# Kernel optimization log

Measured on AMD Instinct MI355X. Metric: run time of the kernel, lower is better.

## Reference

```python
import jax, jax.numpy as jnp
import numpy as np

IN_DIM, D, B, N = 6, 256, 2048, 100  # inner_dim=latent_dim=256, max_size=100


def _glorot(key, shape):
    fan = sum(shape)
    return jax.random.uniform(key, shape, jnp.float32, -1.0, 1.0) * np.sqrt(6.0 / fan)


def setup_inputs() -> dict:
    key = jax.random.key(0)
    ks = jax.random.split(key, 16)
    inp = {
        "x": jax.random.normal(ks[0], (B, N, IN_DIM), jnp.float32),
        "full": 1,
        "remap_w": _glorot(ks[1], (D, IN_DIM)),
        "remap_b": jnp.zeros((D,), jnp.float32),
    }
    for l in range(4):
        k = jax.random.split(ks[2 + l], 3)
        inp[f"w{l+1}"] = _glorot(k[0], (D, D))          # GATConv lin weight (bias=False)
        inp[f"as{l+1}"] = _glorot(k[1], (D,)) * 0.1      # att_src
        inp[f"ad{l+1}"] = _glorot(k[2], (D,)) * 0.1      # att_dst
        inp[f"b{l+1}"] = jnp.zeros((D,), jnp.float32)    # post-aggregation bias
    return inp


def _gat(h, w, a_src, a_dst, b):
    # Complete digraph with self-loops (full=True path) => dense softmax attention.
    g = jnp.einsum("bnd,od->bno", h, w)                  # [B,N,D] transformed nodes
    s_src = jnp.einsum("bno,o->bn", g, a_src)            # score of node as source j
    s_dst = jnp.einsum("bno,o->bn", g, a_dst)            # score of node as target i
    logits = jax.nn.leaky_relu(s_dst[:, :, None] + s_src[:, None, :], 0.2)  # [B,i,j]
    attn = jax.nn.softmax(logits, axis=-1)               # softmax over sources per target
    return jnp.einsum("bij,bjo->bio", attn, g) + b


def reference(x, full, remap_w, remap_b,
              w1, as1, ad1, b1, w2, as2, ad2, b2,
              w3, as3, ad3, b3, w4, as4, ad4, b4):
    h = jax.nn.relu(jnp.einsum("bni,oi->bno", x, remap_w) + remap_b)
    h = jax.nn.relu(_gat(h, w1, as1, ad1, b1) + h)
    h = jax.nn.relu(_gat(h, w2, as2, ad2, b2) + h)
    h = jax.nn.relu(_gat(h, w3, as3, ad3, b3) + h)
    h = _gat(h, w4, as4, ad4, b4)
    return h
```

## Files before the change

### kernel.cpp

```cpp
#include <hip/hip_runtime.h>
#include <hip/hip_bf16.h>


typedef __attribute__((ext_vector_type(8))) short bf16x8;
typedef __attribute__((ext_vector_type(4))) short bf16x4;
typedef __attribute__((ext_vector_type(4))) float f32x4;

__device__ __forceinline__ float bf2f(unsigned short u) {
    return __uint_as_float(((unsigned)u) << 16);
}
__device__ __forceinline__ short f2bfs(float f) {
    __hip_bfloat16 h = __float2bfloat16(f);
    return *reinterpret_cast<short*>(&h);
}

#define HS_OFF 0
#define GT_OFF 57344
#define P_OFF  122880
#define SS_OFF 151552
#define SD_OFF 152000
#define X_OFF  152448
#define SMEM_BYTES 154848

__device__ __forceinline__ int hs_addr(int row, int col) {
    return HS_OFF + row * 512 + ((col * 2) ^ ((row & 7) << 4));
}
__device__ __forceinline__ int gt_addr(int o, int n) {
    return GT_OFF + o * 256 + ((n * 2) ^ ((o & 7) << 4));
}
__device__ __forceinline__ int p_addr(int i, int j) {
    return P_OFF + i * 256 + ((j * 2) ^ ((i & 7) << 4));
}

struct LayerPtrs {
    const float* w[4];
    const float* bias[4];
};
struct PrepPtrs {
    const float* w[4];
    const float* as_[4];
    const float* ad_[4];
};

__global__ __launch_bounds__(256) void prep_kernel(PrepPtrs p, unsigned short* wsd) {
    const int l = blockIdx.x;
    const int d = threadIdx.x;
    __shared__ float As[256], Ad[256];
    As[d] = p.as_[l][d];
    Ad[d] = p.ad_[l][d];
    __syncthreads();
    const float* W = p.w[l];
    float s1 = 0.f, s2 = 0.f;
    for (int o = 0; o < 256; ++o) {
        float wv = W[o * 256 + d];
        s1 = fmaf(wv, As[o], s1);
        s2 = fmaf(wv, Ad[o], s2);
    }
    wsd[l * 512 + d]       = (unsigned short)f2bfs(s1);
    wsd[l * 512 + 256 + d] = (unsigned short)f2bfs(s2);
}

__global__ __launch_bounds__(512) void geom_kernel(
    const float* __restrict__ x,
    const float* __restrict__ remap_w,
    const float* __restrict__ remap_b,
    LayerPtrs lp,
    const unsigned short* __restrict__ wsd,
    float* __restrict__ out)
{
    extern __shared__ char smem[];
    const int tid  = threadIdx.x;
    const int lane = tid & 63;
    const int wv   = tid >> 6;
    const int c    = lane & 15;
    const int q    = lane >> 4;
    const int b    = blockIdx.x;

    for (int off = tid * 16; off < (P_OFF + 28672) - GT_OFF; off += 512 * 16) {
        *(f32x4*)(smem + GT_OFF + off) = f32x4{0.f, 0.f, 0.f, 0.f};
    }
    float* Xs = (float*)(smem + X_OFF);
    const float* xb = x + (size_t)b * 600;
    for (int s = tid; s < 600; s += 512) Xs[s] = xb[s];
    __syncthreads();

    {
        const int o = tid & 255, half = tid >> 8;
        float rw[6];
#pragma unroll
        for (int i = 0; i < 6; ++i) rw[i] = remap_w[o * 6 + i];
        const float rb = remap_b[o];
        for (int n = half * 56; n < half * 56 + 56; ++n) {
            float v = 0.f;
            if (n < 100) {
                v = rb;
#pragma unroll
                for (int i = 0; i < 6; ++i) v = fmaf(Xs[n * 6 + i], rw[i], v);
                v = fmaxf(v, 0.f);
            }
            *(unsigned short*)(smem + hs_addr(n, o)) = (unsigned short)f2bfs(v);
        }
    }

    float res[7][4][2];

    for (int l = 0; l < 4; ++l) {
        __syncthreads();
        const float* W = lp.w[l];
        const int nt0 = 2 * wv, nt1 = 2 * wv + 1;

        {
            bf16x8 wf0[8], wf1[8];
            const float* p0 = W + (nt0 * 16 + c) * 256 + q * 8;
            const float* p1 = W + (nt1 * 16 + c) * 256 + q * 8;
#pragma unroll
            for (int kk = 0; kk < 8; ++kk) {
                f32x4 lo0 = *(const f32x4*)(p0 + kk * 32);
                f32x4 hi0 = *(const f32x4*)(p0 + kk * 32 + 4);
                f32x4 lo1 = *(const f32x4*)(p1 + kk * 32);
                f32x4 hi1 = *(const f32x4*)(p1 + kk * 32 + 4);
                bf16x8 w0, w1;
#pragma unroll
                for (int j = 0; j < 4; ++j) {
                    w0[j]     = f2bfs(lo0[j]);
                    w0[4 + j] = f2bfs(hi0[j]);
                    w1[j]     = f2bfs(lo1[j]);
                    w1[4 + j] = f2bfs(hi1[j]);
                }
                wf0[kk] = w0;
                wf1[kk] = w1;
            }
            for (int mt = 0; mt < 7; ++mt) {
                f32x4 a0e = {0,0,0,0}, a0o = {0,0,0,0}, a1e = {0,0,0,0}, a1o = {0,0,0,0};
#pragma unroll
                for (int kk = 0; kk < 8; kk += 2) {
                    bf16x8 afe = *(const bf16x8*)(smem + hs_addr(mt * 16 + c, kk * 32 + q * 8));
                    bf16x8 afo = *(const bf16x8*)(smem + hs_addr(mt * 16 + c, (kk + 1) * 32 + q * 8));
                    a0e = __builtin_amdgcn_mfma_f32_16x16x32_bf16(afe, wf0[kk],     a0e, 0, 0, 0);
                    a1e = __builtin_amdgcn_mfma_f32_16x16x32_bf16(afe, wf1[kk],     a1e, 0, 0, 0);
                    a0o = __builtin_amdgcn_mfma_f32_16x16x32_bf16(afo, wf0[kk + 1], a0o, 0, 0, 0);
                    a1o = __builtin_amdgcn_mfma_f32_16x16x32_bf16(afo, wf1[kk + 1], a1o, 0, 0, 0);
                }
                f32x4 a0 = a0e + a0o, a1 = a1e + a1o;
                bf16x4 g0, g1;
#pragma unroll
                for (int j = 0; j < 4; ++j) {
                    g0[j] = f2bfs(a0[j]);
                    g1[j] = f2bfs(a1[j]);
                }
                *(bf16x4*)(smem + gt_addr(nt0 * 16 + c, mt * 16 + q * 4)) = g0;
                *(bf16x4*)(smem + gt_addr(nt1 * 16 + c, mt * 16 + q * 4)) = g1;
            }
            if (wv < 7) {
                const unsigned short* wsp = wsd + l * 512 + q * 8;
                const unsigned short* wdp = wsp + 256;
                f32x4 sa = {0,0,0,0};
#pragma unroll
                for (int kk = 0; kk < 8; ++kk) {
                    bf16x8 af = *(const bf16x8*)(smem + hs_addr(wv * 16 + c, kk * 32 + q * 8));
                    bf16x8 bs = *(const bf16x8*)(wsp + kk * 32);
                    bf16x8 bd = *(const bf16x8*)(wdp + kk * 32);
                    bf16x8 bz = {0,0,0,0,0,0,0,0};
                    bf16x8 bb = (c == 0) ? bs : ((c == 1) ? bd : bz);
                    sa = __builtin_amdgcn_mfma_f32_16x16x32_bf16(af, bb, sa, 0, 0, 0);
                }
                if (c < 2) {
                    float* dst = (float*)(smem + (c == 0 ? SS_OFF : SD_OFF));
#pragma unroll
                    for (int j = 0; j < 4; ++j) dst[wv * 16 + q * 4 + j] = sa[j];
                }
            }
        }
        __syncthreads();

        {
            const int i = tid >> 2, sq = tid & 3;
            if (i < 100) {
                const float sd = ((float*)(smem + SD_OFF))[i];
                const float* Ssf = (const float*)(smem + SS_OFF);
                float vals[4][8];
                float mx = -1e30f;
#pragma unroll
                for (int t = 0; t < 4; ++t) {
                    const int blk = t * 4 + sq;
#pragma unroll
                    for (int e = 0; e < 8; ++e) {
                        const int j = blk * 8 + e;
                        float v;
                        if (j < 100) {
                            float z = sd + Ssf[j];
                            v = (z > 0.f) ? z : 0.2f * z;
                        } else {
                            v = -1e30f;
                        }
                        vals[t][e] = v;
                        mx = fmaxf(mx, v);
                    }
                }
                mx = fmaxf(mx, __shfl_xor(mx, 1, 4));
                mx = fmaxf(mx, __shfl_xor(mx, 2, 4));
                float sum = 0.f;
#pragma unroll
                for (int t = 0; t < 4; ++t)
#pragma unroll
                    for (int e = 0; e < 8; ++e) {
                        float ev = __expf(vals[t][e] - mx);
                        vals[t][e] = ev;
                        sum += ev;
                    }
                sum += __shfl_xor(sum, 1, 4);
                sum += __shfl_xor(sum, 2, 4);
                const float inv = 1.f / sum;
#pragma unroll
                for (int t = 0; t < 4; ++t) {
                    const int blk = t * 4 + sq;
                    bf16x8 pv;
#pragma unroll
                    for (int e = 0; e < 8; ++e) pv[e] = f2bfs(vals[t][e] * inv);
                    *(bf16x8*)(smem + p_addr(i, blk * 8)) = pv;
                }
            }
        }
        __syncthreads();

        {
            const float* bias = lp.bias[l];
            const float b0 = bias[nt0 * 16 + c];
            const float b1 = bias[nt1 * 16 + c];
#pragma unroll
            for (int mt = 0; mt < 7; ++mt) {
                f32x4 a0e = {0,0,0,0}, a0o = {0,0,0,0}, a1e = {0,0,0,0}, a1o = {0,0,0,0};
#pragma unroll
                for (int kk = 0; kk < 4; kk += 2) {
                    bf16x8 afe = *(const bf16x8*)(smem + p_addr(mt * 16 + c, kk * 32 + q * 8));
                    bf16x8 afo = *(const bf16x8*)(smem + p_addr(mt * 16 + c, (kk + 1) * 32 + q * 8));
                    bf16x8 g0e = *(const bf16x8*)(smem + gt_addr(nt0 * 16 + c, kk * 32 + q * 8));
                    bf16x8 g1e = *(const bf16x8*)(smem + gt_addr(nt1 * 16 + c, kk * 32 + q * 8));
                    bf16x8 g0o = *(const bf16x8*)(smem + gt_addr(nt0 * 16 + c, (kk + 1) * 32 + q * 8));
                    bf16x8 g1o = *(const bf16x8*)(smem + gt_addr(nt1 * 16 + c, (kk + 1) * 32 + q * 8));
                    a0e = __builtin_amdgcn_mfma_f32_16x16x32_bf16(afe, g0e, a0e, 0, 0, 0);
                    a1e = __builtin_amdgcn_mfma_f32_16x16x32_bf16(afe, g1e, a1e, 0, 0, 0);
                    a0o = __builtin_amdgcn_mfma_f32_16x16x32_bf16(afo, g0o, a0o, 0, 0, 0);
                    a1o = __builtin_amdgcn_mfma_f32_16x16x32_bf16(afo, g1o, a1o, 0, 0, 0);
                }
                f32x4 a0 = a0e + a0o, a1 = a1e + a1o;
                const int row = mt * 16 + q * 4;
                if (l < 3) {
#pragma unroll
                    for (int j = 0; j < 4; ++j) {
                        {
                            const int ad = hs_addr(row + j, nt0 * 16 + c);
                            float r = (l == 0) ? bf2f(*(unsigned short*)(smem + ad))
                                               : res[mt][j][0];
                            float v = fmaxf(a0[j] + b0 + r, 0.f);
                            res[mt][j][0] = v;
                            *(unsigned short*)(smem + ad) = (unsigned short)f2bfs(v);
                        }
                        {
                            const int ad = hs_addr(row + j, nt1 * 16 + c);
                            float r = (l == 0) ? bf2f(*(unsigned short*)(smem + ad))
                                               : res[mt][j][1];
                            float v = fmaxf(a1[j] + b1 + r, 0.f);
                            res[mt][j][1] = v;
                            *(unsigned short*)(smem + ad) = (unsigned short)f2bfs(v);
                        }
                    }
                } else {
                    float* ob = out + (size_t)b * 25600;
#pragma unroll
                    for (int j = 0; j < 4; ++j) {
                        if (row + j < 100) {
                            ob[(row + j) * 256 + nt0 * 16 + c] = a0[j] + b0;
                            ob[(row + j) * 256 + nt1 * 16 + c] = a1[j] + b1;
                        }
                    }
                }
            }
        }
    }
}

extern "C" void kernel_launch(void* const* d_in, const int* in_sizes, int n_in,
                              void* d_out, int out_size, void* d_ws, size_t ws_size,
                              hipStream_t stream) {
    const float* x       = (const float*)d_in[0];
    const float* remap_w = (const float*)d_in[2];
    const float* remap_b = (const float*)d_in[3];
    PrepPtrs pp;
    LayerPtrs lp;
    for (int l = 0; l < 4; ++l) {
        lp.w[l]    = pp.w[l]   = (const float*)d_in[4 + 4 * l];
        pp.as_[l]  = (const float*)d_in[5 + 4 * l];
        pp.ad_[l]  = (const float*)d_in[6 + 4 * l];
        lp.bias[l] = (const float*)d_in[7 + 4 * l];
    }
    unsigned short* wsd = (unsigned short*)d_ws;

    prep_kernel<<<4, 256, 0, stream>>>(pp, wsd);

    (void)hipFuncSetAttribute(reinterpret_cast<const void*>(geom_kernel),
                              hipFuncAttributeMaxDynamicSharedMemorySize, SMEM_BYTES);
    geom_kernel<<<2048, 512, SMEM_BYTES, stream>>>(x, remap_w, remap_b, lp, wsd,
                                                   (float*)d_out);
}
```

Before: 808.9 us.

## Double block to 1024 threads with one feature tile per wave

```diff
diff --git a/kernel.cpp b/kernel.cpp
--- a/kernel.cpp
+++ b/kernel.cpp
@@ -15,12 +15,11 @@
 }
 
 #define HS_OFF 0
-#define GT_OFF 57344
-#define P_OFF  122880
-#define SS_OFF 151552
-#define SD_OFF 152000
-#define X_OFF  152448
-#define SMEM_BYTES 154848
+#define GT_OFF 51200
+#define P_OFF  116736
+#define SS_OFF 145408
+#define SD_OFF 145856
+#define SMEM_BYTES 146304
 
 __device__ __forceinline__ int hs_addr(int row, int col) {
     return HS_OFF + row * 512 + ((col * 2) ^ ((row & 7) << 4));
@@ -60,7 +59,7 @@
     wsd[l * 512 + 256 + d] = (unsigned short)f2bfs(s2);
 }
 
-__global__ __launch_bounds__(512) void geom_kernel(
+__global__ __launch_bounds__(1024) void geom_kernel(
     const float* __restrict__ x,
     const float* __restrict__ remap_w,
     const float* __restrict__ remap_b,
@@ -75,89 +74,77 @@
     const int c    = lane & 15;
     const int q    = lane >> 4;
     const int b    = blockIdx.x;
-
-    for (int off = tid * 16; off < (P_OFF + 28672) - GT_OFF; off += 512 * 16) {
+    const int ft   = wv;
+
+    for (int off = tid * 16; off < 65536; off += 1024 * 16) {
         *(f32x4*)(smem + GT_OFF + off) = f32x4{0.f, 0.f, 0.f, 0.f};
     }
-    float* Xs = (float*)(smem + X_OFF);
-    const float* xb = x + (size_t)b * 600;
-    for (int s = tid; s < 600; s += 512) Xs[s] = xb[s];
-    __syncthreads();
 
     {
-        const int o = tid & 255, half = tid >> 8;
+        const int o = tid & 255, quarter = tid >> 8;
         float rw[6];
 #pragma unroll
         for (int i = 0; i < 6; ++i) rw[i] = remap_w[o * 6 + i];
         const float rb = remap_b[o];
-        for (int n = half * 56; n < half * 56 + 56; ++n) {
-            float v = 0.f;
-            if (n < 100) {
-                v = rb;
-#pragma unroll
-                for (int i = 0; i < 6; ++i) v = fmaf(Xs[n * 6 + i], rw[i], v);
-                v = fmaxf(v, 0.f);
-            }
+        const float* xb = x + (size_t)b * 600;
+        for (int n = quarter * 25; n < quarter * 25 + 25; ++n) {
+            float v = rb;
+#pragma unroll
+            for (int i = 0; i < 6; ++i) v = fmaf(xb[n * 6 + i], rw[i], v);
+            v = fmaxf(v, 0.f);
             *(unsigned short*)(smem + hs_addr(n, o)) = (unsigned short)f2bfs(v);
         }
     }
 
-    float res[7][4][2];
+    float res[7][4];
 
     for (int l = 0; l < 4; ++l) {
         __syncthreads();
         const float* W = lp.w[l];
-        const int nt0 = 2 * wv, nt1 = 2 * wv + 1;
 
         {
-            bf16x8 wf0[8], wf1[8];
-            const float* p0 = W + (nt0 * 16 + c) * 256 + q * 8;
-            const float* p1 = W + (nt1 * 16 + c) * 256 + q * 8;
+            bf16x8 wf[8];
+            const float* wp = W + (ft * 16 + c) * 256 + q * 8;
 #pragma unroll
             for (int kk = 0; kk < 8; ++kk) {
-                f32x4 lo0 = *(const f32x4*)(p0 + kk * 32);
-                f32x4 hi0 = *(const f32x4*)(p0 + kk * 32 + 4);
-                f32x4 lo1 = *(const f32x4*)(p1 + kk * 32);
-                f32x4 hi1 = *(const f32x4*)(p1 + kk * 32 + 4);
-                bf16x8 w0, w1;
+                f32x4 lo = *(const f32x4*)(wp + kk * 32);
+                f32x4 hi = *(const f32x4*)(wp + kk * 32 + 4);
+                bf16x8 w0;
 #pragma unroll
                 for (int j = 0; j < 4; ++j) {
-                    w0[j]     = f2bfs(lo0[j]);
-                    w0[4 + j] = f2bfs(hi0[j]);
-                    w1[j]     = f2bfs(lo1[j]);
-                    w1[4 + j] = f2bfs(hi1[j]);
-                }
-                wf0[kk] = w0;
-                wf1[kk] = w1;
-            }
+                    w0[j]     = f2bfs(lo[j]);
+                    w0[4 + j] = f2bfs(hi[j]);
+                }
+                wf[kk] = w0;
+            }
+#pragma unroll
             for (int mt = 0; mt < 7; ++mt) {
-                f32x4 a0e = {0,0,0,0}, a0o = {0,0,0,0}, a1e = {0,0,0,0}, a1o = {0,0,0,0};
+                int r = mt * 16 + c;
+                if (r > 99) r = 99;
+                f32x4 ae = {0,0,0,0}, ao = {0,0,0,0};
 #pragma unroll
                 for (int kk = 0; kk < 8; kk += 2) {
-                    bf16x8 afe = *(const bf16x8*)(smem + hs_addr(mt * 16 + c, kk * 32 + q * 8));
-                    bf16x8 afo = *(const bf16x8*)(smem + hs_addr(mt * 16 + c, (kk + 1) * 32 + q * 8));
-                    a0e = __builtin_amdgcn_mfma_f32_16x16x32_bf16(afe, wf0[kk],     a0e, 0, 0, 0);
-                    a1e = __builtin_amdgcn_mfma_f32_16x16x32_bf16(afe, wf1[kk],     a1e, 0, 0, 0);
-                    a0o = __builtin_amdgcn_mfma_f32_16x16x32_bf16(afo, wf0[kk + 1], a0o, 0, 0, 0);
-                    a1o = __builtin_amdgcn_mfma_f32_16x16x32_bf16(afo, wf1[kk + 1], a1o, 0, 0, 0);
-                }
-                f32x4 a0 = a0e + a0o, a1 = a1e + a1o;
-                bf16x4 g0, g1;
-#pragma unroll
-                for (int j = 0; j < 4; ++j) {
-                    g0[j] = f2bfs(a0[j]);
-                    g1[j] = f2bfs(a1[j]);
-                }
-                *(bf16x4*)(smem + gt_addr(nt0 * 16 + c, mt * 16 + q * 4)) = g0;
-                *(bf16x4*)(smem + gt_addr(nt1 * 16 + c, mt * 16 + q * 4)) = g1;
-            }
-            if (wv < 7) {
+                    bf16x8 afe = *(const bf16x8*)(smem + hs_addr(r, kk * 32 + q * 8));
+                    bf16x8 afo = *(const bf16x8*)(smem + hs_addr(r, (kk + 1) * 32 + q * 8));
+                    ae = __builtin_amdgcn_mfma_f32_16x16x32_bf16(afe, wf[kk],     ae, 0, 0, 0);
+                    ao = __builtin_amdgcn_mfma_f32_16x16x32_bf16(afo, wf[kk + 1], ao, 0, 0, 0);
+                }
+                f32x4 a = ae + ao;
+                bf16x4 g;
+#pragma unroll
+                for (int j = 0; j < 4; ++j) g[j] = f2bfs(a[j]);
+                *(bf16x4*)(smem + gt_addr(ft * 16 + c, mt * 16 + q * 4)) = g;
+            }
+            if (wv >= 9) {
+                const int st = wv - 9;
+                int r = st * 16 + c;
+                if (r > 99) r = 99;
                 const unsigned short* wsp = wsd + l * 512 + q * 8;
                 const unsigned short* wdp = wsp + 256;
                 f32x4 sa = {0,0,0,0};
 #pragma unroll
                 for (int kk = 0; kk < 8; ++kk) {
-                    bf16x8 af = *(const bf16x8*)(smem + hs_addr(wv * 16 + c, kk * 32 + q * 8));
+                    bf16x8 af = *(const bf16x8*)(smem + hs_addr(r, kk * 32 + q * 8));
                     bf16x8 bs = *(const bf16x8*)(wsp + kk * 32);
                     bf16x8 bd = *(const bf16x8*)(wdp + kk * 32);
                     bf16x8 bz = {0,0,0,0,0,0,0,0};
@@ -167,22 +154,22 @@
                 if (c < 2) {
                     float* dst = (float*)(smem + (c == 0 ? SS_OFF : SD_OFF));
 #pragma unroll
-                    for (int j = 0; j < 4; ++j) dst[wv * 16 + q * 4 + j] = sa[j];
+                    for (int j = 0; j < 4; ++j) dst[st * 16 + q * 4 + j] = sa[j];
                 }
             }
         }
         __syncthreads();
 
         {
-            const int i = tid >> 2, sq = tid & 3;
-            if (i < 100) {
+            const int i = tid >> 3, s3 = tid & 7;
+            if (i < 112) {
                 const float sd = ((float*)(smem + SD_OFF))[i];
                 const float* Ssf = (const float*)(smem + SS_OFF);
-                float vals[4][8];
+                float vals[2][8];
                 float mx = -1e30f;
 #pragma unroll
-                for (int t = 0; t < 4; ++t) {
-                    const int blk = t * 4 + sq;
+                for (int t = 0; t < 2; ++t) {
+                    const int blk = t * 8 + s3;
 #pragma unroll
                     for (int e = 0; e < 8; ++e) {
                         const int j = blk * 8 + e;
@@ -197,23 +184,25 @@
                         mx = fmaxf(mx, v);
                     }
                 }
-                mx = fmaxf(mx, __shfl_xor(mx, 1, 4));
-                mx = fmaxf(mx, __shfl_xor(mx, 2, 4));
+                mx = fmaxf(mx, __shfl_xor(mx, 1, 8));
+                mx = fmaxf(mx, __shfl_xor(mx, 2, 8));
+                mx = fmaxf(mx, __shfl_xor(mx, 4, 8));
                 float sum = 0.f;
 #pragma unroll
-                for (int t = 0; t < 4; ++t)
+                for (int t = 0; t < 2; ++t)
 #pragma unroll
                     for (int e = 0; e < 8; ++e) {
                         float ev = __expf(vals[t][e] - mx);
                         vals[t][e] = ev;
                         sum += ev;
                     }
-                sum += __shfl_xor(sum, 1, 4);
-                sum += __shfl_xor(sum, 2, 4);
+                sum += __shfl_xor(sum, 1, 8);
+                sum += __shfl_xor(sum, 2, 8);
+                sum += __shfl_xor(sum, 4, 8);
                 const float inv = 1.f / sum;
 #pragma unroll
-                for (int t = 0; t < 4; ++t) {
-                    const int blk = t * 4 + sq;
+                for (int t = 0; t < 2; ++t) {
+                    const int blk = t * 8 + s3;
                     bf16x8 pv;
 #pragma unroll
                     for (int e = 0; e < 8; ++e) pv[e] = f2bfs(vals[t][e] * inv);
@@ -224,54 +213,41 @@
         __syncthreads();
 
         {
-            const float* bias = lp.bias[l];
-            const float b0 = bias[nt0 * 16 + c];
-            const float b1 = bias[nt1 * 16 + c];
+            const float b0 = lp.bias[l][ft * 16 + c];
+            bf16x8 gf[4];
+#pragma unroll
+            for (int ks = 0; ks < 4; ++ks)
+                gf[ks] = *(const bf16x8*)(smem + gt_addr(ft * 16 + c, ks * 32 + q * 8));
 #pragma unroll
             for (int mt = 0; mt < 7; ++mt) {
-                f32x4 a0e = {0,0,0,0}, a0o = {0,0,0,0}, a1e = {0,0,0,0}, a1o = {0,0,0,0};
-#pragma unroll
-                for (int kk = 0; kk < 4; kk += 2) {
-                    bf16x8 afe = *(const bf16x8*)(smem + p_addr(mt * 16 + c, kk * 32 + q * 8));
-                    bf16x8 afo = *(const bf16x8*)(smem + p_addr(mt * 16 + c, (kk + 1) * 32 + q * 8));
-                    bf16x8 g0e = *(const bf16x8*)(smem + gt_addr(nt0 * 16 + c, kk * 32 + q * 8));
-                    bf16x8 g1e = *(const bf16x8*)(smem + gt_addr(nt1 * 16 + c, kk * 32 + q * 8));
-                    bf16x8 g0o = *(const bf16x8*)(smem + gt_addr(nt0 * 16 + c, (kk + 1) * 32 + q * 8));
-                    bf16x8 g1o = *(const bf16x8*)(smem + gt_addr(nt1 * 16 + c, (kk + 1) * 32 + q * 8));
-                    a0e = __builtin_amdgcn_mfma_f32_16x16x32_bf16(afe, g0e, a0e, 0, 0, 0);
-                    a1e = __builtin_amdgcn_mfma_f32_16x16x32_bf16(afe, g1e, a1e, 0, 0, 0);
-                    a0o = __builtin_amdgcn_mfma_f32_16x16x32_bf16(afo, g0o, a0o, 0, 0, 0);
-                    a1o = __builtin_amdgcn_mfma_f32_16x16x32_bf16(afo, g1o, a1o, 0, 0, 0);
-                }
-                f32x4 a0 = a0e + a0o, a1 = a1e + a1o;
+                f32x4 ae = {0,0,0,0}, ao = {0,0,0,0};
+#pragma unroll
+                for (int ks = 0; ks < 4; ks += 2) {
+                    bf16x8 pe = *(const bf16x8*)(smem + p_addr(mt * 16 + c, ks * 32 + q * 8));
+                    bf16x8 po = *(const bf16x8*)(smem + p_addr(mt * 16 + c, (ks + 1) * 32 + q * 8));
+                    ae = __builtin_amdgcn_mfma_f32_16x16x32_bf16(pe, gf[ks],     ae, 0, 0, 0);
+                    ao = __builtin_amdgcn_mfma_f32_16x16x32_bf16(po, gf[ks + 1], ao, 0, 0, 0);
+                }
+                f32x4 a = ae + ao;
                 const int row = mt * 16 + q * 4;
                 if (l < 3) {
 #pragma unroll
                     for (int j = 0; j < 4; ++j) {
-                        {
-                            const int ad = hs_addr(row + j, nt0 * 16 + c);
+                        if (row + j < 100) {
+                            const int ad = hs_addr(row + j, ft * 16 + c);
                             float r = (l == 0) ? bf2f(*(unsigned short*)(smem + ad))
-                                               : res[mt][j][0];
-                            float v = fmaxf(a0[j] + b0 + r, 0.f);
-                            res[mt][j][0] = v;
+                                               : res[mt][j];
+                            float v = fmaxf(a[j] + b0 + r, 0.f);
+                            res[mt][j] = v;
                             *(unsigned short*)(smem + ad) = (unsigned short)f2bfs(v);
                         }
-                        {
-                            const int ad = hs_addr(row + j, nt1 * 16 + c);
-                            float r = (l == 0) ? bf2f(*(unsigned short*)(smem + ad))
-                                               : res[mt][j][1];
-                            float v = fmaxf(a1[j] + b1 + r, 0.f);
-                            res[mt][j][1] = v;
-                            *(unsigned short*)(smem + ad) = (unsigned short)f2bfs(v);
-                        }
                     }
                 } else {
                     float* ob = out + (size_t)b * 25600;
 #pragma unroll
                     for (int j = 0; j < 4; ++j) {
                         if (row + j < 100) {
-                            ob[(row + j) * 256 + nt0 * 16 + c] = a0[j] + b0;
-                            ob[(row + j) * 256 + nt1 * 16 + c] = a1[j] + b1;
+                            ob[(row + j) * 256 + ft * 16 + c] = a[j] + b0;
                         }
                     }
                 }
@@ -300,6 +276,6 @@
 
     (void)hipFuncSetAttribute(reinterpret_cast<const void*>(geom_kernel),
                               hipFuncAttributeMaxDynamicSharedMemorySize, SMEM_BYTES);
-    geom_kernel<<<2048, 512, SMEM_BYTES, stream>>>(x, remap_w, remap_b, lp, wsd,
-                                                   (float*)d_out);
-}
+    geom_kernel<<<2048, 1024, SMEM_BYTES, stream>>>(x, remap_w, remap_b, lp, wsd,
+                                                    (float*)d_out);
+}
```

Result: slower. 1.245 ms (+53.9%).
